# Kernel optimization log

Hardware: AMD Instinct MI355X
Metric: run time of the kernel (lower is better)

## Reference

```python
import jax, jax.numpy as jnp
import numpy as np


def _leaky(x):
    return jax.nn.leaky_relu(x, 0.01)


def _seq_query(sess_embed, query, batch_idx, B, W1, b1, W2, b2, a, ab):
    # attention weight per node, then segment-sum per session (vectorized torch.split loop)
    q = query[batch_idx]                                   # [T,D]
    w = jax.nn.sigmoid(q @ W1 + b1 + sess_embed @ W2 + b2) @ a + ab  # [T,1]
    return jax.ops.segment_sum(w * sess_embed, batch_idx, num_segments=B)


def setup_inputs() -> dict:
    key = jax.random.key(0)
    ks = jax.random.split(key, 24)
    N, D, B, L, E, G = 50000, 64, 512, 64, 1650000, 2
    T = B * L
    s = 1.0 / float(np.sqrt(D))
    rn = lambda k, sh: jax.random.normal(k, sh, dtype=jnp.float32) * s
    inp = {
        'sess_idx': jax.random.randint(ks[0], (T,), 0, N),
        'edges': jax.random.randint(ks[1], (2, T), 0, T),
        'batch_idx': jnp.repeat(jnp.arange(B, dtype=jnp.int32), L),
        'tar_poi': jax.random.randint(ks[2], (B,), 0, N),
        'y': (jax.random.uniform(ks[3], (B,)) > 0.5).astype(jnp.float32),
        'edge_index': jax.random.randint(ks[4], (2, E), 0, N),
        'dist_vec': jax.random.uniform(ks[5], (E,), dtype=jnp.float32),
        'poi_embed': rn(ks[6], (N, D)),
        'geo_W0': rn(ks[7], (G, D, D)),
        'geo_W1': rn(ks[8], (G, D, D)),
        'ggc_W': rn(ks[9], (D, D)),
        'gru_wih': rn(ks[10], (3 * D, D)),
        'gru_whh': rn(ks[11], (3 * D, D)),
        'gru_bih': jnp.zeros((3 * D,), jnp.float32),
        'gru_bhh': jnp.zeros((3 * D,), jnp.float32),
        'geoq_W1': rn(ks[12], (D, D)), 'geoq_b1': jnp.zeros((D,), jnp.float32),
        'geoq_W2': rn(ks[13], (D, D)), 'geoq_b2': jnp.zeros((D,), jnp.float32),
        'geoq_a': rn(ks[14], (D, 1)), 'geoq_ab': jnp.zeros((1,), jnp.float32),
        'sessq_W1': rn(ks[15], (D, D)), 'sessq_b1': jnp.zeros((D,), jnp.float32),
        'sessq_W2': rn(ks[16], (D, D)), 'sessq_b2': jnp.zeros((D,), jnp.float32),
        'sessq_a': rn(ks[17], (D, 1)), 'sessq_ab': jnp.zeros((1,), jnp.float32),
        'geo_proj': rn(ks[18], (D, D)),
        'sess_proj': rn(ks[19], (D, D)),
        'mlp_W1': rn(ks[20], (4 * D, D)), 'mlp_b1': jnp.zeros((D,), jnp.float32),
        'mlp_W2': rn(ks[21], (D, 1)), 'mlp_b2': jnp.zeros((1,), jnp.float32),
    }
    return inp


def reference(sess_idx, edges, batch_idx, tar_poi, y, edge_index, dist_vec,
              poi_embed, geo_W0, geo_W1, ggc_W, gru_wih, gru_whh, gru_bih, gru_bhh,
              geoq_W1, geoq_b1, geoq_W2, geoq_b2, geoq_a, geoq_ab,
              sessq_W1, sessq_b1, sessq_W2, sessq_b2, sessq_a, sessq_ab,
              geo_proj, sess_proj, mlp_W1, mlp_b1, mlp_W2, mlp_b2):
    N, D = poi_embed.shape
    B = tar_poi.shape[0]
    T = sess_idx.shape[0]
    row, col = edge_index[0], edge_index[1]

    # symmetric degree norm as in Geo_GCN (degree of col)
    deg = jax.ops.segment_sum(jnp.ones_like(dist_vec), col, num_segments=N)
    dinv = jnp.where(deg > 0, deg ** -0.5, 0.0)
    norm = dinv[row] * dinv[col]
    # NOTE: original applies exp(-d**2) twice (once in CTR.forward, once in Geo_GCN)
    dw = jnp.exp(-jnp.exp(-dist_vec ** 2) ** 2)
    val = (dw * norm)[:, None]                              # [E,1]

    geo_feat = poi_embed
    for i in range(geo_W0.shape[0]):
        side = jax.ops.segment_sum(val * geo_feat[col], row, num_segments=N)  # sparse mm
        geo_feat = _leaky(side @ geo_W0[i] + (geo_feat * side) @ geo_W1[i])
        geo_feat = geo_feat / jnp.maximum(
            jnp.linalg.norm(geo_feat, axis=-1, keepdims=True), 1e-12)

    geo_enc = _seq_query(geo_feat[sess_idx], geo_feat[tar_poi], batch_idx, B,
                         geoq_W1, geoq_b1, geoq_W2, geoq_b2, geoq_a, geoq_ab)
    geo_enc_p = geo_enc @ geo_proj

    # Neigh_pooling: mean aggregation at target node
    neigh = jax.ops.segment_sum(poi_embed[row], col, num_segments=N) \
        / jnp.maximum(deg, 1.0)[:, None]
    counts = jax.ops.segment_sum(jnp.ones((T,), poi_embed.dtype), batch_idx,
                                 num_segments=B)[:, None]
    geo_pool = (jax.ops.segment_sum(neigh[sess_idx], batch_idx, num_segments=B)
                / counts) @ geo_proj

    # GatedGraphConv, num_layers=1: sum-aggregate (h W), then GRU cell
    h = poi_embed[sess_idx]
    m = jax.ops.segment_sum((h @ ggc_W)[edges[0]], edges[1], num_segments=T)
    gi = m @ gru_wih.T + gru_bih
    gh = h @ gru_whh.T + gru_bhh
    ir, iz, i_n = jnp.split(gi, 3, axis=-1)
    hr, hz, h_n = jnp.split(gh, 3, axis=-1)
    r = jax.nn.sigmoid(ir + hr)
    z = jax.nn.sigmoid(iz + hz)
    n = jnp.tanh(i_n + r * h_n)
    sess_hidden = _leaky((1.0 - z) * n + z * h)

    sess_enc = _seq_query(sess_hidden, poi_embed[tar_poi], batch_idx, B,
                          sessq_W1, sessq_b1, sessq_W2, sessq_b2, sessq_a, sessq_ab)
    sess_enc_p = sess_enc @ sess_proj
    sess_pool = (jax.ops.segment_sum(poi_embed[sess_idx], batch_idx,
                                     num_segments=B) / counts) @ sess_proj

    bpr = lambda x, pos, neg: jax.nn.softplus((x * neg).sum(-1) - (x * pos).sum(-1))
    con_loss = bpr(geo_enc, geo_pool, sess_pool) + bpr(sess_enc, sess_pool, geo_pool)

    tar_embed = poi_embed[tar_poi]
    tar_geo_embed = geo_feat[tar_poi]
    feats = jnp.concatenate([tar_embed, tar_geo_embed, sess_enc_p, geo_enc_p], axis=-1)
    logits = (_leaky(feats @ mlp_W1 + mlp_b1) @ mlp_W2 + mlp_b2)[:, 0]
    return logits, con_loss, y, tar_embed, tar_geo_embed, geo_enc_p, sess_enc_p
```

## Files before the change

### kernel.cpp

```cpp
#include <hip/hip_runtime.h>
#include <math.h>

#define CDIV(a,b) (((a)+(b)-1)/(b))

__device__ __forceinline__ float wred(float v){
  #pragma unroll
  for (int o = 32; o; o >>= 1) v += __shfl_xor(v, o, 64);
  return v;
}
__device__ __forceinline__ float leakyf(float x){ return x > 0.f ? x : 0.01f * x; }
__device__ __forceinline__ float sigmf(float x){ return 1.f / (1.f + expf(-x)); }
__device__ __forceinline__ float softplusf(float x){
  return fmaxf(x, 0.f) + log1pf(expf(-fabsf(x)));
}

__global__ void k_deg2(const int* __restrict__ row, const int* __restrict__ col,
                       int* __restrict__ deg_row, int* __restrict__ deg_col,
                       int* __restrict__ rank_r, int* __restrict__ rank_c, int E){
  int e = blockIdx.x * blockDim.x + threadIdx.x;
  if (e < E){
    rank_r[e] = atomicAdd(&deg_row[row[e]], 1);
    rank_c[e] = atomicAdd(&deg_col[col[e]], 1);
  }
}

__global__ __launch_bounds__(1024) void k_scan2(const int* __restrict__ in0, int* __restrict__ out0,
                        const int* __restrict__ in1, int* __restrict__ out1,
                        float* __restrict__ dinv, int n){
  __shared__ int wincl[16];
  const int* in  = blockIdx.x ? in1 : in0;
  int* out       = blockIdx.x ? out1 : out0;
  int tid = threadIdx.x, lane = tid & 63, wv = tid >> 6;
  int carry = 0;
  for (int base = 0; base < n; base += 1024){
    int i = base + tid;
    int x = (i < n) ? in[i] : 0;
    int v = x;
    #pragma unroll
    for (int ofs = 1; ofs < 64; ofs <<= 1){
      int t = __shfl_up(v, ofs, 64);
      if (lane >= ofs) v += t;
    }
    if (lane == 63) wincl[wv] = v;
    __syncthreads();
    if (wv == 0 && lane < 16){
      int s = wincl[lane];
      #pragma unroll
      for (int ofs = 1; ofs < 16; ofs <<= 1){
        int t = __shfl_up(s, ofs, 64);
        if (lane >= ofs) s += t;
      }
      wincl[lane] = s;
    }
    __syncthreads();
    int woff = wv ? wincl[wv - 1] : 0;
    if (i < n) out[i] = carry + woff + v - x;
    carry += wincl[15];
    __syncthreads();
  }
  if (tid == 0) out[n] = carry;
  if (blockIdx.x == 1){
    for (int i = tid; i < n; i += 1024){
      int d = in1[i];
      dinv[i] = d > 0 ? 1.f / sqrtf((float)d) : 0.f;
    }
  }
}

__global__ void k_fill2(const int* __restrict__ row, const int* __restrict__ col,
                        const float* __restrict__ dist, const float* __restrict__ dinv,
                        const int* __restrict__ offs_r, const int* __restrict__ rank_r,
                        int2* __restrict__ csr_cv,
                        const int* __restrict__ offs_c, const int* __restrict__ rank_c,
                        int* __restrict__ csr_row, int E){
  int e = blockIdx.x * blockDim.x + threadIdx.x;
  if (e < E){
    int r = row[e], c = col[e];
    int pr = offs_r[r] + rank_r[e];
    float d = dist[e];
    float t = expf(-d * d);
    float dw = expf(-t * t);
    csr_cv[pr] = make_int2(c, __float_as_int(dw * dinv[r] * dinv[c]));
    int pc = offs_c[c] + rank_c[e];
    csr_row[pc] = r;
  }
}

__global__ __launch_bounds__(512) void k_gcn2(const int* __restrict__ offs,
                      const int2* __restrict__ csr_cv,
                      const float* __restrict__ gfeat,
                      const float* __restrict__ W0, const float* __restrict__ W1,
                      float* __restrict__ out, int N){
  __shared__ float lw0[4096], lw1[4096];
  for (int i = threadIdx.x; i < 4096; i += 512){ lw0[i] = W0[i]; lw1[i] = W1[i]; }
  __syncthreads();
  int lane = threadIdx.x & 63, wave = threadIdx.x >> 6;
  int grp = lane >> 4, pos = lane & 15;
  const float4* gf4 = (const float4*)gfeat;
  int wgl = blockIdx.x * 8 + wave;
  int nw = gridDim.x * 8;
  for (int r = wgl; r < N; r += nw){
    int j0 = offs[r], j1 = offs[r + 1];
    float4 s4 = {0.f, 0.f, 0.f, 0.f};
    for (int jb = j0; jb < j1; jb += 64){
      int rem = j1 - jb;
      int cnt = rem < 64 ? rem : 64;
      int jj = jb + lane;
      int2 cv = make_int2(0, 0);
      if (jj < j1) cv = csr_cv[jj];
      int myc = cv.x; float myv = __int_as_float(cv.y);
      int rounds = (cnt + 3) >> 2;
      int kk = 0;
      for (; kk + 4 <= rounds; kk += 4){
        int e0 = (kk+0)*4 + grp, e1 = (kk+1)*4 + grp,
            e2 = (kk+2)*4 + grp, e3 = (kk+3)*4 + grp;
        int   c0 = __shfl(myc, e0, 64), c1 = __shfl(myc, e1, 64),
              c2 = __shfl(myc, e2, 64), c3 = __shfl(myc, e3, 64);
        float v0 = __shfl(myv, e0, 64), v1 = __shfl(myv, e1, 64),
              v2 = __shfl(myv, e2, 64), v3 = __shfl(myv, e3, 64);
        float4 f0 = gf4[(long)c0 * 16 + pos];
        float4 f1 = gf4[(long)c1 * 16 + pos];
        float4 f2 = gf4[(long)c2 * 16 + pos];
        float4 f3 = gf4[(long)c3 * 16 + pos];
        s4.x += v0*f0.x; s4.y += v0*f0.y; s4.z += v0*f0.z; s4.w += v0*f0.w;
        s4.x += v1*f1.x; s4.y += v1*f1.y; s4.z += v1*f1.z; s4.w += v1*f1.w;
        s4.x += v2*f2.x; s4.y += v2*f2.y; s4.z += v2*f2.z; s4.w += v2*f2.w;
        s4.x += v3*f3.x; s4.y += v3*f3.y; s4.z += v3*f3.z; s4.w += v3*f3.w;
      }
      for (; kk < rounds; kk++){
        int e = kk*4 + grp;
        int c = __shfl(myc, e, 64);
        float v = __shfl(myv, e, 64);
        float4 f = gf4[(long)c * 16 + pos];
        s4.x += v*f.x; s4.y += v*f.y; s4.z += v*f.z; s4.w += v*f.w;
      }
    }
    #pragma unroll
    for (int m = 16; m <= 32; m <<= 1){
      s4.x += __shfl_xor(s4.x, m, 64);
      s4.y += __shfl_xor(s4.y, m, 64);
      s4.z += __shfl_xor(s4.z, m, 64);
      s4.w += __shfl_xor(s4.w, m, 64);
    }
    int src = lane >> 2, cc = lane & 3;
    float sx = __shfl(s4.x, src, 64);
    float sy = __shfl(s4.y, src, 64);
    float sz = __shfl(s4.z, src, 64);
    float sw = __shfl(s4.w, src, 64);
    float s = (cc == 0) ? sx : (cc == 1) ? sy : (cc == 2) ? sz : sw;

    float g = gfeat[(long)r * 64 + lane];
    float acc = 0.f;
    #pragma unroll
    for (int k = 0; k < 64; k++){
      float sk = __shfl(s, k, 64);
      float gk = __shfl(g, k, 64);
      acc += sk * lw0[k * 64 + lane] + gk * sk * lw1[k * 64 + lane];
    }
    float x = leakyf(acc);
    float nrm = sqrtf(wred(x * x));
    out[(long)r * 64 + lane] = x / fmaxf(nrm, 1e-12f);
  }
}

__global__ __launch_bounds__(256) void k_pool_gather(const int* __restrict__ offs,
                      const int* __restrict__ csr_row,
                      const float* __restrict__ poi, float* __restrict__ neigh, int N){
  int lane = threadIdx.x & 63, wave = threadIdx.x >> 6;
  int grp = lane >> 4, pos = lane & 15;
  const float4* poi4 = (const float4*)poi;
  int wgl = blockIdx.x * 4 + wave;
  int nw = gridDim.x * 4;
  for (int n = wgl; n < N; n += nw){
    int j0 = offs[n], j1 = offs[n + 1];
    float4 s4 = {0.f, 0.f, 0.f, 0.f};
    for (int jb = j0; jb < j1; jb += 64){
      int rem = j1 - jb;
      int cnt = rem < 64 ? rem : 64;
      int jj = jb + lane;
      int myc = 0; float myw = 0.f;
      if (jj < j1){ myc = csr_row[jj]; myw = 1.f; }
      int rounds = (cnt + 3) >> 2;
      int kk = 0;
      for (; kk + 4 <= rounds; kk += 4){
        int e0 = (kk+0)*4 + grp, e1 = (kk+1)*4 + grp,
            e2 = (kk+2)*4 + grp, e3 = (kk+3)*4 + grp;
        int   c0 = __shfl(myc, e0, 64), c1 = __shfl(myc, e1, 64),
              c2 = __shfl(myc, e2, 64), c3 = __shfl(myc, e3, 64);
        float v0 = __shfl(myw, e0, 64), v1 = __shfl(myw, e1, 64),
              v2 = __shfl(myw, e2, 64), v3 = __shfl(myw, e3, 64);
        float4 f0 = poi4[(long)c0 * 16 + pos];
        float4 f1 = poi4[(long)c1 * 16 + pos];
        float4 f2 = poi4[(long)c2 * 16 + pos];
        float4 f3 = poi4[(long)c3 * 16 + pos];
        s4.x += v0*f0.x; s4.y += v0*f0.y; s4.z += v0*f0.z; s4.w += v0*f0.w;
        s4.x += v1*f1.x; s4.y += v1*f1.y; s4.z += v1*f1.z; s4.w += v1*f1.w;
        s4.x += v2*f2.x; s4.y += v2*f2.y; s4.z += v2*f2.z; s4.w += v2*f2.w;
        s4.x += v3*f3.x; s4.y += v3*f3.y; s4.z += v3*f3.z; s4.w += v3*f3.w;
      }
      for (; kk < rounds; kk++){
        int e = kk*4 + grp;
        int c = __shfl(myc, e, 64);
        float v = __shfl(myw, e, 64);
        float4 f = poi4[(long)c * 16 + pos];
        s4.x += v*f.x; s4.y += v*f.y; s4.z += v*f.z; s4.w += v*f.w;
      }
    }
    #pragma unroll
    for (int m = 16; m <= 32; m <<= 1){
      s4.x += __shfl_xor(s4.x, m, 64);
      s4.y += __shfl_xor(s4.y, m, 64);
      s4.z += __shfl_xor(s4.z, m, 64);
      s4.w += __shfl_xor(s4.w, m, 64);
    }
    int src = lane >> 2, cc = lane & 3;
    float sx = __shfl(s4.x, src, 64);
    float sy = __shfl(s4.y, src, 64);
    float sz = __shfl(s4.z, src, 64);
    float sw = __shfl(s4.w, src, 64);
    float s = (cc == 0) ? sx : (cc == 1) ? sy : (cc == 2) ? sz : sw;
    float inv = 1.f / fmaxf((float)(j1 - j0), 1.f);
    neigh[(long)n * 64 + lane] = s * inv;
  }
}

template<bool GATHER>
__global__ __launch_bounds__(256) void k_gemm64(const float* __restrict__ X, const int* __restrict__ ridx,
                         const float* __restrict__ W, const float* __restrict__ bias,
                         float* __restrict__ Y, int M){
  __shared__ float lw[4096];
  for (int i = threadIdx.x; i < 4096; i += 256) lw[i] = W[i];
  __syncthreads();
  int lane = threadIdx.x & 63, wave = threadIdx.x >> 6;
  int wgl = blockIdx.x * 4 + wave;
  int nw = gridDim.x * 4;
  for (int r = wgl; r < M; r += nw){
    long src = GATHER ? (long)ridx[r] : (long)r;
    float x = X[src * 64 + lane];
    float acc = bias ? bias[lane] : 0.f;
    #pragma unroll
    for (int k = 0; k < 64; k++) acc += __shfl(x, k, 64) * lw[k * 64 + lane];
    Y[(long)r * 64 + lane] = acc;
  }
}

template<bool GATHER_S>
__global__ __launch_bounds__(256) void k_seqq(const float* __restrict__ sbase, const int* __restrict__ sidx,
                       const float* __restrict__ qbase, const int* __restrict__ tar,
                       const float* __restrict__ W1, const float* __restrict__ b1,
                       const float* __restrict__ W2, const float* __restrict__ b2,
                       const float* __restrict__ a, const float* __restrict__ ab,
                       float* __restrict__ out, int L){
  __shared__ float lw1[4096], lw2[4096], la[64], lb[64];
  __shared__ float red[4][64];
  int tid = threadIdx.x;
  for (int i = tid; i < 4096; i += 256){ lw1[i] = W1[i]; lw2[i] = W2[i]; }
  if (tid < 64){ la[tid] = a[tid]; lb[tid] = b1[tid] + b2[tid]; }
  __syncthreads();
  int lane = tid & 63, wave = tid >> 6;
  int b = blockIdx.x;
  float q = qbase[(long)tar[b] * 64 + lane];
  float ab0 = ab[0];
  float hq = lb[lane];
  #pragma unroll
  for (int k = 0; k < 64; k++) hq += __shfl(q, k, 64) * lw1[k * 64 + lane];
  float acc = 0.f;
  for (int tl = wave; tl < L; tl += 4){
    int t = b * L + tl;
    long srow = GATHER_S ? (long)sidx[t] : (long)t;
    float s = sbase[srow * 64 + lane];
    float h = hq;
    #pragma unroll
    for (int k = 0; k < 64; k++) h += __shfl(s, k, 64) * lw2[k * 64 + lane];
    float sg = sigmf(h);
    float w = wred(sg * la[lane]) + ab0;
    acc += w * s;
  }
  red[wave][lane] = acc;
  __syncthreads();
  if (tid < 64)
    out[(long)b * 64 + tid] = red[0][tid] + red[1][tid] + red[2][tid] + red[3][tid];
}

__global__ __launch_bounds__(256) void k_pool(const float* __restrict__ neigh, const float* __restrict__ poi,
                       const int* __restrict__ sidx, float* __restrict__ p1,
                       float* __restrict__ p2, int L){
  __shared__ float r1[4][64], r2[4][64];
  int tid = threadIdx.x, lane = tid & 63, wave = tid >> 6, b = blockIdx.x;
  float a1 = 0.f, a2 = 0.f;
  for (int tl = wave; tl < L; tl += 4){
    long idx = sidx[b * L + tl];
    a1 += neigh[idx * 64 + lane];
    a2 += poi[idx * 64 + lane];
  }
  r1[wave][lane] = a1; r2[wave][lane] = a2;
  __syncthreads();
  float inv = 1.f / (float)L;
  if (tid < 64){
    p1[(long)b * 64 + tid] = (r1[0][tid] + r1[1][tid] + r1[2][tid] + r1[3][tid]) * inv;
    p2[(long)b * 64 + tid] = (r2[0][tid] + r2[1][tid] + r2[2][tid] + r2[3][tid]) * inv;
  }
}

__global__ void k_edge_scatter(const int* __restrict__ e0, const int* __restrict__ e1,
                               const float* __restrict__ hw, float* __restrict__ m, int T){
  long gid = (long)blockIdx.x * blockDim.x + threadIdx.x;
  if (gid >= (long)T * 64) return;
  int e = (int)(gid >> 6), c = (int)(gid & 63);
  atomicAdd(&m[(long)e1[e] * 64 + c], hw[(long)e0[e] * 64 + c]);
}

__global__ __launch_bounds__(256) void k_gi(const float* __restrict__ m,
                     const float* __restrict__ wih, const float* __restrict__ bih,
                     float* __restrict__ gi, int T){
  __shared__ float lw[64 * 193];
  __shared__ float lb[192];
  int tid = threadIdx.x, lane = tid & 63, wave = tid >> 6;
  if (tid < 192) lb[tid] = bih[tid];
  for (int idx = tid; idx < 192 * 64; idx += 256){
    int j = idx >> 6, k = idx & 63;
    lw[k * 193 + j] = wih[idx];
  }
  __syncthreads();
  int r0 = blockIdx.x * 4 + wave, nw = gridDim.x * 4;
  for (int t = r0; t < T; t += nw){
    float x = m[(long)t * 64 + lane];
    float a0 = lb[lane], a1 = lb[64 + lane], a2 = lb[128 + lane];
    #pragma unroll
    for (int k = 0; k < 64; k++){
      float xk = __shfl(x, k, 64);
      a0 += xk * lw[k * 193 + lane];
      a1 += xk * lw[k * 193 + 64 + lane];
      a2 += xk * lw[k * 193 + 128 + lane];
    }
    gi[(long)t * 192 + lane] = a0;
    gi[(long)t * 192 + 64 + lane] = a1;
    gi[(long)t * 192 + 128 + lane] = a2;
  }
}

__global__ __launch_bounds__(256) void k_gru2(const float* __restrict__ gi,
                       const float* __restrict__ poi, const int* __restrict__ sidx,
                       const float* __restrict__ whh, const float* __restrict__ bhh,
                       float* __restrict__ out, int T){
  __shared__ float lw[64 * 193];
  __shared__ float lb[192];
  int tid = threadIdx.x, lane = tid & 63, wave = tid >> 6;
  if (tid < 192) lb[tid] = bhh[tid];
  for (int idx = tid; idx < 192 * 64; idx += 256){
    int j = idx >> 6, k = idx & 63;
    lw[k * 193 + j] = whh[idx];
  }
  __syncthreads();
  int r0 = blockIdx.x * 4 + wave, nw = gridDim.x * 4;
  for (int t = r0; t < T; t += nw){
    float h = poi[(long)sidx[t] * 64 + lane];
    float b0 = lb[lane], b1 = lb[64 + lane], b2 = lb[128 + lane];
    #pragma unroll
    for (int k = 0; k < 64; k++){
      float hk = __shfl(h, k, 64);
      b0 += hk * lw[k * 193 + lane];
      b1 += hk * lw[k * 193 + 64 + lane];
      b2 += hk * lw[k * 193 + 128 + lane];
    }
    float r = sigmf(gi[(long)t * 192 + lane] + b0);
    float z = sigmf(gi[(long)t * 192 + 64 + lane] + b1);
    float n = tanhf(gi[(long)t * 192 + 128 + lane] + r * b2);
    float nh = (1.f - z) * n + z * h;
    out[(long)t * 64 + lane] = leakyf(nh);
  }
}

__global__ __launch_bounds__(64) void k_final(
    const float* __restrict__ poi, const float* __restrict__ gf,
    const int* __restrict__ tar,
    const float* __restrict__ geo_enc, const float* __restrict__ sess_enc,
    const float* __restrict__ gpool, const float* __restrict__ spool,
    const float* __restrict__ mW1, const float* __restrict__ mb1,
    const float* __restrict__ mW2, const float* __restrict__ mb2,
    const float* __restrict__ y, float* __restrict__ out, int B){
  int b = blockIdx.x, c = threadIdx.x;
  long tp = tar[b];
  long offT = 3L * B, offG = 3L * B + (long)B * 64;
  long offGP = 3L * B + 2L * B * 64, offSP = 3L * B + 3L * B * 64;
  float f0 = poi[tp * 64 + c];
  float f1 = gf[tp * 64 + c];
  float f2 = out[offSP + (long)b * 64 + c];
  float f3 = out[offGP + (long)b * 64 + c];
  float ge = geo_enc[(long)b * 64 + c], se = sess_enc[(long)b * 64 + c];
  float gp = gpool[(long)b * 64 + c], sp = spool[(long)b * 64 + c];
  float d1 = wred(ge * sp);
  float d2 = wred(ge * gp);
  float d3 = wred(se * gp);
  float d4 = wred(se * sp);
  float con = softplusf(d1 - d2) + softplusf(d3 - d4);
  float acc = mb1[c];
  #pragma unroll
  for (int k = 0; k < 64; k++){
    acc += __shfl(f0, k, 64) * mW1[k * 64 + c];
    acc += __shfl(f1, k, 64) * mW1[(64 + k) * 64 + c];
    acc += __shfl(f2, k, 64) * mW1[(128 + k) * 64 + c];
    acc += __shfl(f3, k, 64) * mW1[(192 + k) * 64 + c];
  }
  float hid = leakyf(acc);
  float lsum = wred(hid * mW2[c]);
  if (c == 0){
    out[b] = lsum + mb2[0];
    out[B + b] = con;
    out[2L * B + b] = y[b];
  }
  out[offT + (long)b * 64 + c] = f0;
  out[offG + (long)b * 64 + c] = f1;
}

extern "C" void kernel_launch(void* const* d_in, const int* in_sizes, int n_in,
                              void* d_out, int out_size, void* d_ws, size_t ws_size,
                              hipStream_t stream){
  const int*   sess_idx = (const int*)d_in[0];
  const int*   edges    = (const int*)d_in[1];
  const int*   tar_poi  = (const int*)d_in[3];
  const float* y        = (const float*)d_in[4];
  const int*   eidx     = (const int*)d_in[5];
  const float* dist     = (const float*)d_in[6];
  const float* poi      = (const float*)d_in[7];
  const float* geoW0    = (const float*)d_in[8];
  const float* geoW1    = (const float*)d_in[9];
  const float* ggcW     = (const float*)d_in[10];
  const float* wih      = (const float*)d_in[11];
  const float* whh      = (const float*)d_in[12];
  const float* bih      = (const float*)d_in[13];
  const float* bhh      = (const float*)d_in[14];
  const float* geoqW1   = (const float*)d_in[15];
  const float* geoqb1   = (const float*)d_in[16];
  const float* geoqW2   = (const float*)d_in[17];
  const float* geoqb2   = (const float*)d_in[18];
  const float* geoqa    = (const float*)d_in[19];
  const float* geoqab   = (const float*)d_in[20];
  const float* sessqW1  = (const float*)d_in[21];
  const float* sessqb1  = (const float*)d_in[22];
  const float* sessqW2  = (const float*)d_in[23];
  const float* sessqb2  = (const float*)d_in[24];
  const float* sessqa   = (const float*)d_in[25];
  const float* sessqab  = (const float*)d_in[26];
  const float* geo_proj = (const float*)d_in[27];
  const float* sess_proj= (const float*)d_in[28];
  const float* mW1      = (const float*)d_in[29];
  const float* mb1      = (const float*)d_in[30];
  const float* mW2      = (const float*)d_in[31];
  const float* mb2      = (const float*)d_in[32];

  const int T = in_sizes[0];
  const int B = in_sizes[3];
  const int E = in_sizes[5] / 2;
  const int N = in_sizes[7] / 64;
  const int G = in_sizes[8] / 4096;
  const int L = T / B;
  const int* erow = eidx;
  const int* ecol = eidx + E;
  const int* e0 = edges;
  const int* e1 = edges + T;

  char* w = (char*)d_ws;
  size_t off = 0;
  auto nxt = [&](size_t bytes)->void*{
    void* p = w + off; off = (off + bytes + 255) & ~(size_t)255; return p;
  };
  int*   deg_row = (int*)  nxt((size_t)N * 4);
  int*   deg_col = (int*)  nxt((size_t)N * 4);
  int*   offs_r  = (int*)  nxt((size_t)(N + 1) * 4);
  int*   offs_c  = (int*)  nxt((size_t)(N + 1) * 4);
  float* dinv    = (float*)nxt((size_t)N * 4);
  float* gf1     = (float*)nxt((size_t)N * 256);
  float* geo_enc = (float*)nxt((size_t)B * 256);
  float* sess_enc= (float*)nxt((size_t)B * 256);
  float* p1      = (float*)nxt((size_t)B * 256);
  float* p2      = (float*)nxt((size_t)B * 256);
  float* gpool   = (float*)nxt((size_t)B * 256);
  float* spool   = (float*)nxt((size_t)B * 256);
  float* gf0     = (float*)nxt((size_t)N * 256);
  int2*  csr_cv  = (int2*) nxt((size_t)E * 8);
  int*   csr_row = (int*)  nxt((size_t)E * 4);
  float* poolbuf = (float*)nxt((size_t)N * 256);
  float* hw      = (float*)nxt((size_t)T * 256);
  float* gi      = gf0;
  float* neigh   = poolbuf;
  float* mbuf    = poolbuf;
  float* sessh   = hw;
  int*   rank_r  = (int*)poolbuf;
  int*   rank_c  = rank_r + E;
  float* outf    = (float*)d_out;

  const long offGP = 3L * B + 2L * B * 64;
  const long offSP = 3L * B + 3L * B * 64;

  hipMemsetAsync(deg_row, 0, (size_t)N * 4, stream);
  hipMemsetAsync(deg_col, 0, (size_t)N * 4, stream);
  k_deg2<<<CDIV(E,256),256,0,stream>>>(erow, ecol, deg_row, deg_col, rank_r, rank_c, E);
  k_scan2<<<2,1024,0,stream>>>(deg_row, offs_r, deg_col, offs_c, dinv, N);
  k_fill2<<<CDIV(E,256),256,0,stream>>>(erow, ecol, dist, dinv,
                                        offs_r, rank_r, csr_cv,
                                        offs_c, rank_c, csr_row, E);

  const float* cur = poi;
  float* nextb = (G & 1) ? gf1 : gf0;
  for (int g = 0; g < G; g++){
    k_gcn2<<<1024,512,0,stream>>>(offs_r, csr_cv, cur,
                                  geoW0 + (size_t)g * 4096, geoW1 + (size_t)g * 4096,
                                  nextb, N);
    cur = nextb;
    nextb = (nextb == gf0) ? gf1 : gf0;
  }
  const float* gf = cur;

  k_seqq<true><<<B,256,0,stream>>>(gf, sess_idx, gf, tar_poi,
                                   geoqW1, geoqb1, geoqW2, geoqb2, geoqa, geoqab,
                                   geo_enc, L);
  k_gemm64<false><<<CDIV(B,4),256,0,stream>>>(geo_enc, nullptr, geo_proj, nullptr,
                                              outf + offGP, B);

  k_pool_gather<<<2048,256,0,stream>>>(offs_c, csr_row, poi, neigh, N);
  k_pool<<<B,256,0,stream>>>(neigh, poi, sess_idx, p1, p2, L);
  k_gemm64<false><<<CDIV(B,4),256,0,stream>>>(p1, nullptr, geo_proj, nullptr, gpool, B);
  k_gemm64<false><<<CDIV(B,4),256,0,stream>>>(p2, nullptr, sess_proj, nullptr, spool, B);

  k_gemm64<true><<<2048,256,0,stream>>>(poi, sess_idx, ggcW, nullptr, hw, T);
  hipMemsetAsync(mbuf, 0, (size_t)T * 256, stream);
  k_edge_scatter<<<(int)CDIV((long)T*64,256),256,0,stream>>>(e0, e1, hw, mbuf, T);
  k_gi<<<1024,256,0,stream>>>(mbuf, wih, bih, gi, T);
  k_gru2<<<1024,256,0,stream>>>(gi, poi, sess_idx, whh, bhh, sessh, T);

  k_seqq<false><<<B,256,0,stream>>>(sessh, nullptr, poi, tar_poi,
                                    sessqW1, sessqb1, sessqW2, sessqb2, sessqa, sessqab,
                                    sess_enc, L);
  k_gemm64<false><<<CDIV(B,4),256,0,stream>>>(sess_enc, nullptr, sess_proj, nullptr,
                                              outf + offSP, B);

  k_final<<<B,64,0,stream>>>(poi, gf, tar_poi, geo_enc, sess_enc, gpool, spool,
                             mW1, mb1, mW2, mb2, y, outf, B);
}
```

Baseline: 822.2 us.

## Replace edge atomic scatter with CSR gather and fuse projection GEMMs

The per-channel atomicAdd scatter of session edge messages is replaced by building a small CSR over destination nodes (degree count, single-block scan, fill). The GRU input kernel now gathers and sums neighbour rows directly, which removes the memset and the atomic traffic on a T×64 buffer. Separately, the 64×64 projection GEMMs are folded into the seq-query and pooling kernels, removing four small launches and their intermediate buffers. The cost is three extra small kernels plus a serial single-block scan over T entries, and the projection weights now have to be loaded into shared memory in every block.

```diff
diff --git a/kernel.cpp b/kernel.cpp
--- a/kernel.cpp
+++ b/kernel.cpp
@@ -65,6 +65,53 @@
       dinv[i] = d > 0 ? 1.f / sqrtf((float)d) : 0.f;
     }
   }
+}
+
+__global__ __launch_bounds__(1024) void k_scanT(const int* __restrict__ in,
+                                                int* __restrict__ out, int n){
+  __shared__ int wincl[16];
+  int tid = threadIdx.x, lane = tid & 63, wv = tid >> 6;
+  int carry = 0;
+  for (int base = 0; base < n; base += 1024){
+    int i = base + tid;
+    int x = (i < n) ? in[i] : 0;
+    int v = x;
+    #pragma unroll
+    for (int ofs = 1; ofs < 64; ofs <<= 1){
+      int t = __shfl_up(v, ofs, 64);
+      if (lane >= ofs) v += t;
+    }
+    if (lane == 63) wincl[wv] = v;
+    __syncthreads();
+    if (wv == 0 && lane < 16){
+      int s = wincl[lane];
+      #pragma unroll
+      for (int ofs = 1; ofs < 16; ofs <<= 1){
+        int t = __shfl_up(s, ofs, 64);
+        if (lane >= ofs) s += t;
+      }
+      wincl[lane] = s;
+    }
+    __syncthreads();
+    int woff = wv ? wincl[wv - 1] : 0;
+    if (i < n) out[i] = carry + woff + v - x;
+    carry += wincl[15];
+    __syncthreads();
+  }
+  if (tid == 0) out[n] = carry;
+}
+
+__global__ void k_degT(const int* __restrict__ e1, int* __restrict__ degt,
+                       int* __restrict__ rankt, int T){
+  int e = blockIdx.x * blockDim.x + threadIdx.x;
+  if (e < T) rankt[e] = atomicAdd(&degt[e1[e]], 1);
+}
+
+__global__ void k_fillT(const int* __restrict__ e0, const int* __restrict__ e1,
+                        const int* __restrict__ offs, const int* __restrict__ rankt,
+                        int* __restrict__ csr_src, int T){
+  int e = blockIdx.x * blockDim.x + threadIdx.x;
+  if (e < T) csr_src[offs[e1[e]] + rankt[e]] = e0[e];
 }
 
 __global__ void k_fill2(const int* __restrict__ row, const int* __restrict__ col,
@@ -250,9 +297,11 @@
                        const float* __restrict__ W1, const float* __restrict__ b1,
                        const float* __restrict__ W2, const float* __restrict__ b2,
                        const float* __restrict__ a, const float* __restrict__ ab,
-                       float* __restrict__ out, int L){
+                       const float* __restrict__ proj,
+                       float* __restrict__ enc_out, float* __restrict__ proj_out, int L){
   __shared__ float lw1[4096], lw2[4096], la[64], lb[64];
   __shared__ float red[4][64];
+  __shared__ float encs[64];
   int tid = threadIdx.x;
   for (int i = tid; i < 4096; i += 256){ lw1[i] = W1[i]; lw2[i] = W2[i]; }
   if (tid < 64){ la[tid] = a[tid]; lb[tid] = b1[tid] + b2[tid]; }
@@ -278,15 +327,31 @@
   }
   red[wave][lane] = acc;
   __syncthreads();
-  if (tid < 64)
-    out[(long)b * 64 + tid] = red[0][tid] + red[1][tid] + red[2][tid] + red[3][tid];
+  if (tid < 64){
+    float e = red[0][tid] + red[1][tid] + red[2][tid] + red[3][tid];
+    encs[tid] = e;
+    enc_out[(long)b * 64 + tid] = e;
+  }
+  __syncthreads();
+  for (int i = tid; i < 4096; i += 256) lw1[i] = proj[i];
+  __syncthreads();
+  if (tid < 64){
+    float ap = 0.f;
+    #pragma unroll
+    for (int k = 0; k < 64; k++) ap += encs[k] * lw1[k * 64 + tid];
+    proj_out[(long)b * 64 + tid] = ap;
+  }
 }
 
 __global__ __launch_bounds__(256) void k_pool(const float* __restrict__ neigh, const float* __restrict__ poi,
-                       const int* __restrict__ sidx, float* __restrict__ p1,
-                       float* __restrict__ p2, int L){
+                       const int* __restrict__ sidx,
+                       const float* __restrict__ projG, const float* __restrict__ projS,
+                       float* __restrict__ gpool, float* __restrict__ spool, int L){
+  __shared__ float lwg[4096], lws[4096];
   __shared__ float r1[4][64], r2[4][64];
+  __shared__ float p1s[64], p2s[64];
   int tid = threadIdx.x, lane = tid & 63, wave = tid >> 6, b = blockIdx.x;
+  for (int i = tid; i < 4096; i += 256){ lwg[i] = projG[i]; lws[i] = projS[i]; }
   float a1 = 0.f, a2 = 0.f;
   for (int tl = wave; tl < L; tl += 4){
     long idx = sidx[b * L + tl];
@@ -295,22 +360,26 @@
   }
   r1[wave][lane] = a1; r2[wave][lane] = a2;
   __syncthreads();
-  float inv = 1.f / (float)L;
   if (tid < 64){
-    p1[(long)b * 64 + tid] = (r1[0][tid] + r1[1][tid] + r1[2][tid] + r1[3][tid]) * inv;
-    p2[(long)b * 64 + tid] = (r2[0][tid] + r2[1][tid] + r2[2][tid] + r2[3][tid]) * inv;
-  }
-}
-
-__global__ void k_edge_scatter(const int* __restrict__ e0, const int* __restrict__ e1,
-                               const float* __restrict__ hw, float* __restrict__ m, int T){
-  long gid = (long)blockIdx.x * blockDim.x + threadIdx.x;
-  if (gid >= (long)T * 64) return;
-  int e = (int)(gid >> 6), c = (int)(gid & 63);
-  atomicAdd(&m[(long)e1[e] * 64 + c], hw[(long)e0[e] * 64 + c]);
-}
-
-__global__ __launch_bounds__(256) void k_gi(const float* __restrict__ m,
+    float inv = 1.f / (float)L;
+    p1s[tid] = (r1[0][tid] + r1[1][tid] + r1[2][tid] + r1[3][tid]) * inv;
+    p2s[tid] = (r2[0][tid] + r2[1][tid] + r2[2][tid] + r2[3][tid]) * inv;
+  }
+  __syncthreads();
+  if (tid < 64){
+    float ag = 0.f, as = 0.f;
+    #pragma unroll
+    for (int k = 0; k < 64; k++){
+      ag += p1s[k] * lwg[k * 64 + tid];
+      as += p2s[k] * lws[k * 64 + tid];
+    }
+    gpool[(long)b * 64 + tid] = ag;
+    spool[(long)b * 64 + tid] = as;
+  }
+}
+
+__global__ __launch_bounds__(256) void k_gi(const float* __restrict__ hw,
+                     const int* __restrict__ offs_t, const int* __restrict__ csr_src,
                      const float* __restrict__ wih, const float* __restrict__ bih,
                      float* __restrict__ gi, int T){
   __shared__ float lw[64 * 193];
@@ -324,7 +393,10 @@
   __syncthreads();
   int r0 = blockIdx.x * 4 + wave, nw = gridDim.x * 4;
   for (int t = r0; t < T; t += nw){
-    float x = m[(long)t * 64 + lane];
+    int j0 = offs_t[t], j1 = offs_t[t + 1];
+    float x = 0.f;
+    for (int j = j0; j < j1; j++)
+      x += hw[(long)csr_src[j] * 64 + lane];
     float a0 = lb[lane], a1 = lb[64 + lane], a2 = lb[128 + lane];
     #pragma unroll
     for (int k = 0; k < 64; k++){
@@ -470,11 +542,13 @@
   int*   offs_r  = (int*)  nxt((size_t)(N + 1) * 4);
   int*   offs_c  = (int*)  nxt((size_t)(N + 1) * 4);
   float* dinv    = (float*)nxt((size_t)N * 4);
+  int*   degt    = (int*)  nxt((size_t)T * 4);
+  int*   rankt   = (int*)  nxt((size_t)T * 4);
+  int*   offs_t  = (int*)  nxt((size_t)(T + 1) * 4);
+  int*   csr_src = (int*)  nxt((size_t)T * 4);
   float* gf1     = (float*)nxt((size_t)N * 256);
   float* geo_enc = (float*)nxt((size_t)B * 256);
   float* sess_enc= (float*)nxt((size_t)B * 256);
-  float* p1      = (float*)nxt((size_t)B * 256);
-  float* p2      = (float*)nxt((size_t)B * 256);
   float* gpool   = (float*)nxt((size_t)B * 256);
   float* spool   = (float*)nxt((size_t)B * 256);
   float* gf0     = (float*)nxt((size_t)N * 256);
@@ -484,7 +558,6 @@
   float* hw      = (float*)nxt((size_t)T * 256);
   float* gi      = gf0;
   float* neigh   = poolbuf;
-  float* mbuf    = poolbuf;
   float* sessh   = hw;
   int*   rank_r  = (int*)poolbuf;
   int*   rank_c  = rank_r + E;
@@ -514,26 +587,23 @@
 
   k_seqq<true><<<B,256,0,stream>>>(gf, sess_idx, gf, tar_poi,
                                    geoqW1, geoqb1, geoqW2, geoqb2, geoqa, geoqab,
-                                   geo_enc, L);
-  k_gemm64<false><<<CDIV(B,4),256,0,stream>>>(geo_enc, nullptr, geo_proj, nullptr,
-                                              outf + offGP, B);
+                                   geo_proj, geo_enc, outf + offGP, L);
 
   k_pool_gather<<<2048,256,0,stream>>>(offs_c, csr_row, poi, neigh, N);
-  k_pool<<<B,256,0,stream>>>(neigh, poi, sess_idx, p1, p2, L);
-  k_gemm64<false><<<CDIV(B,4),256,0,stream>>>(p1, nullptr, geo_proj, nullptr, gpool, B);
-  k_gemm64<false><<<CDIV(B,4),256,0,stream>>>(p2, nullptr, sess_proj, nullptr, spool, B);
+  k_pool<<<B,256,0,stream>>>(neigh, poi, sess_idx, geo_proj, sess_proj,
+                             gpool, spool, L);
 
   k_gemm64<true><<<2048,256,0,stream>>>(poi, sess_idx, ggcW, nullptr, hw, T);
-  hipMemsetAsync(mbuf, 0, (size_t)T * 256, stream);
-  k_edge_scatter<<<(int)CDIV((long)T*64,256),256,0,stream>>>(e0, e1, hw, mbuf, T);
-  k_gi<<<1024,256,0,stream>>>(mbuf, wih, bih, gi, T);
+  hipMemsetAsync(degt, 0, (size_t)T * 4, stream);
+  k_degT<<<CDIV(T,256),256,0,stream>>>(e1, degt, rankt, T);
+  k_scanT<<<1,1024,0,stream>>>(degt, offs_t, T);
+  k_fillT<<<CDIV(T,256),256,0,stream>>>(e0, e1, offs_t, rankt, csr_src, T);
+  k_gi<<<1024,256,0,stream>>>(hw, offs_t, csr_src, wih, bih, gi, T);
   k_gru2<<<1024,256,0,stream>>>(gi, poi, sess_idx, whh, bhh, sessh, T);
 
   k_seqq<false><<<B,256,0,stream>>>(sessh, nullptr, poi, tar_poi,
                                     sessqW1, sessqb1, sessqW2, sessqb2, sessqa, sessqab,
-                                    sess_enc, L);
-  k_gemm64<false><<<CDIV(B,4),256,0,stream>>>(sess_enc, nullptr, sess_proj, nullptr,
-                                              outf + offSP, B);
+                                    sess_proj, sess_enc, outf + offSP, L);
 
   k_final<<<B,64,0,stream>>>(poi, gf, tar_poi, geo_enc, sess_enc, gpool, spool,
                              mW1, mb1, mW2, mb2, y, outf, B);
```

Measured after the change: 853.6 us. +3.8%, slower.
